# Kernel optimization log

Hardware: AMD Instinct MI355X
Metric: run time of the kernel (lower is better)

Reference implementation:

```python
import jax, jax.numpy as jnp
import numpy as np

N, LT, LV, D, H = 4, 1024, 1024, 1024, 16
HD = D // H
EPS = 1e-12


def layernorm(x, w, b):
    u = x.mean(-1, keepdims=True)
    s = ((x - u) ** 2).mean(-1, keepdims=True)
    return w * (x - u) / jnp.sqrt(s + EPS) + b


def attention(q_in, k_in, v_in, mask, qw, qb, kw, kb, vw, vb):
    # mask: (N, Lq_or_1, Lk) float in {0,1}; torch Linear is x @ W.T + b
    def heads(x, w, b):
        y = x @ w.T + b
        return y.reshape(y.shape[0], y.shape[1], H, HD).transpose(0, 2, 1, 3)  # (N,H,L,hd)
    q, k, v = heads(q_in, qw, qb), heads(k_in, kw, kb), heads(v_in, vw, vb)
    scores = jnp.einsum('bhqd,bhkd->bhqk', q, k) / np.sqrt(HD).astype(np.float32)
    scores = scores + (1.0 - mask[:, None]) * (-10000.0)
    probs = jax.nn.softmax(scores, axis=-1)  # dropout is identity in eval
    ctx = jnp.einsum('bhqk,bhkd->bhqd', probs, v)
    return ctx.transpose(0, 2, 1, 3).reshape(q_in.shape[0], q_in.shape[1], D)


def setup_inputs() -> dict:
    key = jax.random.key(0)
    ks = jax.random.split(key, 16)
    inp = {
        'dec_hidden_states': jax.random.normal(ks[0], (N, LT, D), jnp.float32),
        'enc_outputs': jax.random.normal(ks[1], (N, LV, D), jnp.float32),
        'dec_mask': jnp.ones((N, LT), jnp.float32),
        'enc_mask': jnp.ones((N, LV), jnp.float32),
    }
    wnames = ['sa_qw', 'sa_kw', 'sa_vw', 'ca_qw', 'ca_kw', 'ca_vw', 'out_w']
    for i, n in enumerate(wnames):
        inp[n] = jax.random.normal(ks[2 + i], (D, D), jnp.float32) * 0.02
    for n in ['sa_qb', 'sa_kb', 'sa_vb', 'ca_qb', 'ca_kb', 'ca_vb', 'out_b', 'n1_b', 'n2_b', 'out_ln_b']:
        inp[n] = jnp.zeros((D,), jnp.float32)
    for n in ['n1_w', 'n2_w', 'out_ln_w']:
        inp[n] = jnp.ones((D,), jnp.float32)
    return inp


def reference(dec_hidden_states, enc_outputs, dec_mask, enc_mask,
              sa_qw, sa_qb, sa_kw, sa_kb, sa_vw, sa_vb, n1_w, n1_b,
              ca_qw, ca_qb, ca_kw, ca_kb, ca_vw, ca_vb, n2_w, n2_b,
              out_w, out_b, out_ln_w, out_ln_b):
    Lt = dec_mask.shape[1]
    # diagonal_mask=True: causal tril combined with padding mask
    self_mask = dec_mask[:, None, :] * jnp.tril(jnp.ones((Lt, Lt), dec_mask.dtype))  # (N,Lt,Lt)
    a = attention(dec_hidden_states, dec_hidden_states, dec_hidden_states, self_mask,
                  sa_qw, sa_qb, sa_kw, sa_kb, sa_vw, sa_vb)
    a = layernorm(a + dec_hidden_states, n1_w, n1_b)
    c = attention(a, enc_outputs, enc_outputs, enc_mask[:, None, :],
                  ca_qw, ca_qb, ca_kw, ca_kb, ca_vw, ca_vb)
    c = layernorm(a + c, n2_w, n2_b)
    # BertOutput called as output(x, x): dense, residual, LN (dropout = identity)
    h = c @ out_w.T + out_b
    return layernorm(h + c, out_ln_w, out_ln_b)
```

## Files before the change

kernel.cpp:

```cpp
#include <hip/hip_runtime.h>
#include <cstdint>
#include <cstddef>

typedef __bf16 bf16x8 __attribute__((ext_vector_type(8)));
typedef float  floatx4 __attribute__((ext_vector_type(4)));
typedef unsigned short ushortx8 __attribute__((ext_vector_type(8)));
typedef unsigned short ushortx4 __attribute__((ext_vector_type(4)));

#define MFMA16(a, b, c) __builtin_amdgcn_mfma_f32_16x16x32_bf16((a), (b), (c), 0, 0, 0)

__device__ inline unsigned short f2bf(float f) {
    unsigned int u = __float_as_uint(f);
    unsigned int r = (u + 0x7fffu + ((u >> 16) & 1u)) >> 16;
    return (unsigned short)r;
}

struct Src2 { const float* p[2]; };
__global__ __launch_bounds__(256) void k_x2_to_bf16(Src2 s2, unsigned short* __restrict__ dst) {
    int i = blockIdx.x * 256 + threadIdx.x;
    const float* src = s2.p[i >> 19];
    int off = i & 524287;
    const float4* s = (const float4*)src + (size_t)off * 2;
    float4 x0 = s[0], x1 = s[1];
    ushortx8 o;
    o[0] = f2bf(x0.x); o[1] = f2bf(x0.y); o[2] = f2bf(x0.z); o[3] = f2bf(x0.w);
    o[4] = f2bf(x1.x); o[5] = f2bf(x1.y); o[6] = f2bf(x1.z); o[7] = f2bf(x1.w);
    *((ushortx8*)dst + i) = o;
}
struct Src7 { const float* p[7]; };
__global__ __launch_bounds__(256) void k_w7_to_bf16(Src7 s7, unsigned short* __restrict__ dst) {
    int i = blockIdx.x * 256 + threadIdx.x;
    const float* src = s7.p[i >> 17];
    int off = i & 131071;
    const float4* s = (const float4*)src + (size_t)off * 2;
    float4 x0 = s[0], x1 = s[1];
    ushortx8 o;
    o[0] = f2bf(x0.x); o[1] = f2bf(x0.y); o[2] = f2bf(x0.z); o[3] = f2bf(x0.w);
    o[4] = f2bf(x1.x); o[5] = f2bf(x1.y); o[6] = f2bf(x1.z); o[7] = f2bf(x1.w);
    *((ushortx8*)dst + i) = o;
}

template <int MODE>
__global__ __launch_bounds__(256) void k_gemm_bias(const unsigned short* __restrict__ A,
                                                   const unsigned short* __restrict__ A2,
                                                   const unsigned short* __restrict__ W,
                                                   const float* __restrict__ bias0,
                                                   const float* __restrict__ bias1,
                                                   const float* __restrict__ bias2,
                                                   void* __restrict__ d0,
                                                   void* __restrict__ d1,
                                                   void* __restrict__ d2,
                                                   int K) {
    __shared__ __align__(16) unsigned short As[128 * 32];
    __shared__ __align__(16) unsigned short Bs[128 * 32];
    const int tid = threadIdx.x;
    const int wave = tid >> 6, lane = tid & 63;
    const int quad = lane >> 4, l15 = lane & 15;
    const int wm = wave >> 1, wn = wave & 1;
    const int m0 = blockIdx.x * 128, n0 = blockIdx.y * 128;
    const int sect_blk = n0 >> 10;

    const unsigned short* Ause = (MODE == 4 && sect_blk != 0) ? A2 : A;

    const size_t rowbytes = (size_t)K * 2;
    const int idx0 = tid, idx1 = 256 + tid;
    const int rA0 = idx0 >> 2, cb0 = (idx0 & 3) << 4;
    const int rA1 = idx1 >> 2, cb1 = (idx1 & 3) << 4;
    const char* gA0 = (const char*)Ause + (size_t)(m0 + rA0) * rowbytes + cb0;
    const char* gA1 = (const char*)Ause + (size_t)(m0 + rA1) * rowbytes + cb1;
    const char* gB0 = (const char*)W + (size_t)(n0 + rA0) * rowbytes + cb0;
    const char* gB1 = (const char*)W + (size_t)(n0 + rA1) * rowbytes + cb1;

    int4 pa0 = *(const int4*)gA0, pa1 = *(const int4*)gA1;
    int4 pb0 = *(const int4*)gB0, pb1 = *(const int4*)gB1;

    floatx4 acc[4][4] = {};

    const int KT = K >> 5;
    for (int kt = 0; kt < KT; ++kt) {
        __syncthreads();
        ((int4*)As)[idx0] = pa0; ((int4*)As)[idx1] = pa1;
        ((int4*)Bs)[idx0] = pb0; ((int4*)Bs)[idx1] = pb1;
        __syncthreads();
        if (kt + 1 < KT) {
            gA0 += 64; gA1 += 64; gB0 += 64; gB1 += 64;
            pa0 = *(const int4*)gA0; pa1 = *(const int4*)gA1;
            pb0 = *(const int4*)gB0; pb1 = *(const int4*)gB1;
        }
        bf16x8 af[4], bfr[4];
        const char* Asb = (const char*)As;
        const char* Bsb = (const char*)Bs;
#pragma unroll
        for (int r = 0; r < 4; ++r)
            af[r] = *(const bf16x8*)(Asb + ((wm * 64 + r * 16 + l15) * 64 + quad * 16));
#pragma unroll
        for (int c = 0; c < 4; ++c)
            bfr[c] = *(const bf16x8*)(Bsb + ((wn * 64 + c * 16 + l15) * 64 + quad * 16));
#pragma unroll
        for (int r = 0; r < 4; ++r)
#pragma unroll
            for (int c = 0; c < 4; ++c)
                acc[r][c] = MFMA16(af[r], bfr[c], acc[r][c]);
    }

#pragma unroll
    for (int c = 0; c < 4; ++c) {
        int col = n0 + wn * 64 + c * 16 + l15;
        int sect = col >> 10, cc = col & 1023;
        float bv;
        if (MODE == 3) bv = bias0[col];
        else bv = (sect == 0 ? bias0 : (sect == 1 ? bias1 : bias2))[cc];
        int h = cc >> 6, d = cc & 63;
#pragma unroll
        for (int r = 0; r < 4; ++r) {
            int mrow = m0 + wm * 64 + r * 16 + quad * 4;
#pragma unroll
            for (int i = 0; i < 4; ++i) {
                float v = acc[r][c][i] + bv;
                int row = mrow + i;
                if (MODE == 3) {
                    ((float*)d0)[(size_t)row * 1024 + col] = v;
                } else {
                    int b = row >> 10, l = row & 1023;
                    unsigned short* base = (unsigned short*)(sect == 0 ? d0 : (sect == 1 ? d1 : d2));
                    bool isV = (sect == 2);
                    size_t off;
                    if (isV) {
                        int kk = l & 31;
                        int kperm = ((kk & 15) << 1) | (kk >> 4);
                        off = (size_t)(b * 16 + h) * 65536 + (size_t)(l >> 5) * 2048 + d * 32 + kperm;
                    } else {
                        off = ((size_t)(b * 16 + h) * 1024 + l) * 64 + d;
                    }
                    base[off] = f2bf(v);
                }
            }
        }
    }
}

__global__ __launch_bounds__(256, 2) void k_flash_attn(const unsigned short* __restrict__ Qp,
                                                       const unsigned short* __restrict__ Kp,
                                                       const unsigned short* __restrict__ Vp,
                                                       const float* __restrict__ mask,
                                                       float* __restrict__ ctx,
                                                       int causal) {
    const int L = 1024, D = 1024;
    const float SC = 0.18033688011112042f;
    int f = blockIdx.x;
    int g = f >> 6;
    int bh = (f & 7) + (g << 3);
    int qt = ((f >> 3) + g) & 7;
    int h = bh & 15, b = bh >> 4;
    int tid = threadIdx.x;
    int wave = tid >> 6, lane = tid & 63, quad = lane >> 4, l15 = lane & 15;
    int qbase = qt * 128 + wave * 32;

    __shared__ __align__(16) unsigned short Ks[4096];
    __shared__ __align__(16) unsigned short Vs[5120];
    __shared__ float penf[1024];
    __shared__ __align__(16) unsigned short Plds[4 * 1280];

    {
        float4 mv = ((const float4*)(mask + b * L))[tid];
        float4 pv;
        pv.x = (1.0f - mv.x) * -14426.950408889634f;
        pv.y = (1.0f - mv.y) * -14426.950408889634f;
        pv.z = (1.0f - mv.z) * -14426.950408889634f;
        pv.w = (1.0f - mv.w) * -14426.950408889634f;
        ((float4*)penf)[tid] = pv;
    }

    const unsigned short* Qh = Qp + ((size_t)(b * 16 + h) * 1024 + qbase) * 64;
    bf16x8 qf[2][2];
#pragma unroll
    for (int qh = 0; qh < 2; ++qh) {
        qf[qh][0] = *(const bf16x8*)(Qh + (qh * 16 + l15) * 64 + quad * 8);
        qf[qh][1] = *(const bf16x8*)(Qh + (qh * 16 + l15) * 64 + 32 + quad * 8);
    }

    const char* Kh = (const char*)(Kp + (size_t)(b * 16 + h) * 65536);
    const char* Vh = (const char*)(Vp + (size_t)(b * 16 + h) * 65536);

    int ktiles = causal ? (2 * qt + 2) : 16;

    char* Ksb = (char*)Ks;
    char* Vsb = (char*)Vs;
    int krow = tid >> 3, kblk = tid & 7;
    int kd0 = krow * 128 + ((kblk ^ (krow & 7)) << 4);
    int kd1 = kd0 + 32 * 128;
    int vd0 = (tid >> 2) * 80 + ((tid & 3) << 4);
    int vd1 = vd0 + 5120;

    int karA[4], karB[4];
#pragma unroll
    for (int r = 0; r < 4; ++r) {
        int row = r * 16 + l15;
        karA[r] = row * 128 + ((quad ^ (l15 & 7)) << 4);
        karB[r] = row * 128 + (((quad | 4) ^ (l15 & 7)) << 4);
    }
    int var_[8];
#pragma unroll
    for (int s = 0; s < 2; ++s)
#pragma unroll
        for (int fi = 0; fi < 4; ++fi)
            var_[s * 4 + fi] = s * 5120 + (fi * 16 + l15) * 80 + (quad << 4);

    floatx4 O[2][4] = {};
    float lsum[2][4] = {};
    unsigned short* pw = &Plds[wave * 1280];
    unsigned int* pw32 = (unsigned int*)pw;

    int4 ka0 = *(const int4*)(Kh + tid * 16);
    int4 ka1 = *(const int4*)(Kh + 4096 + tid * 16);
    int4 va0 = *(const int4*)(Vh + tid * 16);
    int4 va1 = *(const int4*)(Vh + 4096 + tid * 16);

    for (int kt = 0; kt < ktiles; ++kt) {
        *(int4*)(Ksb + kd0) = ka0;
        *(int4*)(Ksb + kd1) = ka1;
        *(int4*)(Vsb + vd0) = va0;
        *(int4*)(Vsb + vd1) = va1;
        __syncthreads();
        if (kt + 1 < ktiles) {
            const char* Kg = Kh + (size_t)(kt + 1) * 8192;
            const char* Vg = Vh + (size_t)(kt + 1) * 8192;
            ka0 = *(const int4*)(Kg + tid * 16);
            ka1 = *(const int4*)(Kg + 4096 + tid * 16);
            va0 = *(const int4*)(Vg + tid * 16);
            va1 = *(const int4*)(Vg + 4096 + tid * 16);
        }
        int k0 = kt * 64;

        if (!(causal && k0 > qbase + 31)) {
            bf16x8 kA[4], kB[4];
#pragma unroll
            for (int r = 0; r < 4; ++r) {
                kA[r] = *(const bf16x8*)(Ksb + karA[r]);
                kB[r] = *(const bf16x8*)(Ksb + karB[r]);
            }
            bf16x8 vv[8];
#pragma unroll
            for (int s = 0; s < 8; ++s) vv[s] = *(const bf16x8*)(Vsb + var_[s]);
            float pr0 = penf[k0 + l15];
            float pr1 = penf[k0 + 16 + l15];
            float pr2 = penf[k0 + 32 + l15];
            float pr3 = penf[k0 + 48 + l15];

#pragma unroll
            for (int qh = 0; qh < 2; ++qh) {
                int qlo = qbase + qh * 16;
                if (causal && k0 > qlo + 15) continue;
                bool boundary = causal && (k0 + 63 > qlo);

                floatx4 S0 = {}, S1 = {}, S2 = {}, S3 = {};
                S0 = MFMA16(qf[qh][0], kA[0], S0); S0 = MFMA16(qf[qh][1], kB[0], S0);
                S1 = MFMA16(qf[qh][0], kA[1], S1); S1 = MFMA16(qf[qh][1], kB[1], S1);
                S2 = MFMA16(qf[qh][0], kA[2], S2); S2 = MFMA16(qf[qh][1], kB[2], S2);
                S3 = MFMA16(qf[qh][0], kA[3], S3); S3 = MFMA16(qf[qh][1], kB[3], S3);

                int qrow = qlo + quad * 4;
#pragma unroll
                for (int i = 0; i < 4; ++i) {
                    float x0 = fmaf(S0[i], SC, pr0);
                    float x1 = fmaf(S1[i], SC, pr1);
                    float x2 = fmaf(S2[i], SC, pr2);
                    float x3 = fmaf(S3[i], SC, pr3);
                    if (boundary) {
                        int q = qrow + i;
                        x0 = ((k0 + l15) <= q) ? x0 : -50000.0f;
                        x1 = ((k0 + 16 + l15) <= q) ? x1 : -50000.0f;
                        x2 = ((k0 + 32 + l15) <= q) ? x2 : -50000.0f;
                        x3 = ((k0 + 48 + l15) <= q) ? x3 : -50000.0f;
                    }
                    float p0 = __builtin_amdgcn_exp2f(x0);
                    float p1 = __builtin_amdgcn_exp2f(x1);
                    float p2 = __builtin_amdgcn_exp2f(x2);
                    float p3 = __builtin_amdgcn_exp2f(x3);
                    lsum[qh][i] += (p0 + p1) + (p2 + p3);
                    unsigned r0 = __float_as_uint(p0) + 0x8000u;
                    unsigned r1 = __float_as_uint(p1) + 0x8000u;
                    unsigned r2 = __float_as_uint(p2) + 0x8000u;
                    unsigned r3 = __float_as_uint(p3) + 0x8000u;
                    unsigned plo = __builtin_amdgcn_perm(r1, r0, 0x07060302u);
                    unsigned phi = __builtin_amdgcn_perm(r3, r2, 0x07060302u);
                    int ro = (quad * 4 + i) * 20;
                    pw32[ro + l15] = plo;
                    pw32[320 + ro + l15] = phi;
                }
                bf16x8 pa_lo = *(const bf16x8*)(pw + l15 * 40 + quad * 8);
                bf16x8 pa_hi = *(const bf16x8*)(pw + 640 + l15 * 40 + quad * 8);
                O[qh][0] = MFMA16(pa_lo, vv[0], O[qh][0]);
                O[qh][1] = MFMA16(pa_lo, vv[1], O[qh][1]);
                O[qh][2] = MFMA16(pa_lo, vv[2], O[qh][2]);
                O[qh][3] = MFMA16(pa_lo, vv[3], O[qh][3]);
                O[qh][0] = MFMA16(pa_hi, vv[4], O[qh][0]);
                O[qh][1] = MFMA16(pa_hi, vv[5], O[qh][1]);
                O[qh][2] = MFMA16(pa_hi, vv[6], O[qh][2]);
                O[qh][3] = MFMA16(pa_hi, vv[7], O[qh][3]);
            }
        }
        __syncthreads();
    }

#pragma unroll
    for (int qh = 0; qh < 2; ++qh)
#pragma unroll
        for (int i = 0; i < 4; ++i) {
            float l = lsum[qh][i];
            l += __shfl_xor(l, 1);
            l += __shfl_xor(l, 2);
            l += __shfl_xor(l, 4);
            l += __shfl_xor(l, 8);
            float inv = 1.0f / l;
            int q = qbase + qh * 16 + quad * 4 + i;
            float* op = ctx + ((size_t)(b * L + q)) * D + h * 64;
#pragma unroll
            for (int fi = 0; fi < 4; ++fi) op[fi * 16 + l15] = O[qh][fi][i] * inv;
        }
}

__global__ __launch_bounds__(256) void k_add_ln(const float* __restrict__ X,
                                                const float* __restrict__ Y,
                                                const float* __restrict__ w,
                                                const float* __restrict__ bvec,
                                                float* __restrict__ outf,
                                                unsigned short* __restrict__ outbf) {
    int row = blockIdx.x;
    int tid = threadIdx.x;
    float4 x = *((const float4*)(X + (size_t)row * 1024) + tid);
    float4 y = *((const float4*)(Y + (size_t)row * 1024) + tid);
    float v0 = x.x + y.x, v1 = x.y + y.y, v2 = x.z + y.z, v3 = x.w + y.w;
    float s = v0 + v1 + v2 + v3;
    float s2 = v0 * v0 + v1 * v1 + v2 * v2 + v3 * v3;
#pragma unroll
    for (int off = 32; off > 0; off >>= 1) {
        s += __shfl_xor(s, off);
        s2 += __shfl_xor(s2, off);
    }
    __shared__ float red[8];
    int wave = tid >> 6, lane = tid & 63;
    if (lane == 0) { red[wave] = s; red[4 + wave] = s2; }
    __syncthreads();
    s = red[0] + red[1] + red[2] + red[3];
    s2 = red[4] + red[5] + red[6] + red[7];
    float u = s * (1.0f / 1024.0f);
    float var = s2 * (1.0f / 1024.0f) - u * u;
    float r = 1.0f / sqrtf(fmaxf(var, 0.0f) + 1e-12f);
    float4 wv = *((const float4*)w + tid);
    float4 bv = *((const float4*)bvec + tid);
    float o0 = wv.x * (v0 - u) * r + bv.x;
    float o1 = wv.y * (v1 - u) * r + bv.y;
    float o2 = wv.z * (v2 - u) * r + bv.z;
    float o3 = wv.w * (v3 - u) * r + bv.w;
    float4 o = {o0, o1, o2, o3};
    *((float4*)(outf + (size_t)row * 1024) + tid) = o;
    if (outbf) {
        ushortx4 ob;
        ob[0] = f2bf(o0); ob[1] = f2bf(o1); ob[2] = f2bf(o2); ob[3] = f2bf(o3);
        *((ushortx4*)outbf + (size_t)row * 256 + tid) = ob;
    }
}

extern "C" void kernel_launch(void* const* d_in, const int* in_sizes, int n_in,
                              void* d_out, int out_size, void* d_ws, size_t ws_size,
                              hipStream_t stream) {
    (void)in_sizes; (void)n_in; (void)out_size; (void)ws_size;
    const float* dec = (const float*)d_in[0];
    const float* enc = (const float*)d_in[1];
    const float* dec_mask = (const float*)d_in[2];
    const float* enc_mask = (const float*)d_in[3];
    const float* b_saq = (const float*)d_in[11];
    const float* b_sak = (const float*)d_in[12];
    const float* b_sav = (const float*)d_in[13];
    const float* b_caq = (const float*)d_in[14];
    const float* b_cak = (const float*)d_in[15];
    const float* b_cav = (const float*)d_in[16];
    const float* b_out = (const float*)d_in[17];
    const float* n1_b = (const float*)d_in[18];
    const float* n2_b = (const float*)d_in[19];
    const float* oln_b = (const float*)d_in[20];
    const float* n1_w = (const float*)d_in[21];
    const float* n2_w = (const float*)d_in[22];
    const float* oln_w = (const float*)d_in[23];

    char* ws = (char*)d_ws;
    const size_t MB2 = 2097152;
    const size_t ACT_BF = 8388608;
    const size_t ACT_F32 = 16777216;
    unsigned short* Wbf[7];
    for (int i = 0; i < 7; ++i) Wbf[i] = (unsigned short*)(ws + i * MB2);
    size_t off = 7 * MB2;
    unsigned short* Xbf = (unsigned short*)(ws + off); off += ACT_BF;
    unsigned short* Ebf = (unsigned short*)(ws + off); off += ACT_BF;
    unsigned short* Abf = (unsigned short*)(ws + off); off += ACT_BF;
    unsigned short* Cbf = (unsigned short*)(ws + off); off += ACT_BF;
    unsigned short* Qp = (unsigned short*)(ws + off); off += ACT_BF;
    unsigned short* Kp = (unsigned short*)(ws + off); off += ACT_BF;
    unsigned short* Vp = (unsigned short*)(ws + off); off += ACT_BF;
    float* ctx = (float*)(ws + off); off += ACT_F32;
    float* a_f32 = (float*)(ws + off); off += ACT_F32;
    float* c_f32 = (float*)(ws + off); off += ACT_F32;
    float* h_f32 = ctx;
    float* outp = (float*)d_out;

    dim3 blk(256);
    dim3 attn_grid(512);

    Src2 s2; s2.p[0] = dec; s2.p[1] = enc;
    k_x2_to_bf16<<<dim3(4096), blk, 0, stream>>>(s2, Xbf);
    Src7 s7;
    for (int i = 0; i < 7; ++i) s7.p[i] = (const float*)d_in[4 + i];
    k_w7_to_bf16<<<dim3(3584), blk, 0, stream>>>(s7, Wbf[0]);

    k_gemm_bias<0><<<dim3(32, 24), blk, 0, stream>>>(Xbf, Xbf, Wbf[0], b_saq, b_sak, b_sav,
                                                     Qp, Kp, Vp, 1024);
    k_flash_attn<<<attn_grid, blk, 0, stream>>>(Qp, Kp, Vp, dec_mask, ctx, 1);
    k_add_ln<<<dim3(4096), blk, 0, stream>>>(ctx, dec, n1_w, n1_b, a_f32, Abf);

    k_gemm_bias<4><<<dim3(32, 24), blk, 0, stream>>>(Abf, Ebf, Wbf[3], b_caq, b_cak, b_cav,
                                                     Qp, Kp, Vp, 1024);
    k_flash_attn<<<attn_grid, blk, 0, stream>>>(Qp, Kp, Vp, enc_mask, ctx, 0);
    k_add_ln<<<dim3(4096), blk, 0, stream>>>(a_f32, ctx, n2_w, n2_b, c_f32, Cbf);

    k_gemm_bias<3><<<dim3(32, 8), blk, 0, stream>>>(Cbf, Cbf, Wbf[6], b_out, b_out, b_out,
                                                    h_f32, nullptr, nullptr, 1024);
    k_add_ln<<<dim3(4096), blk, 0, stream>>>(h_f32, c_f32, oln_w, oln_b, outp, (unsigned short*)nullptr);
}
```

Baseline: 337.6 us.

## Double GEMM K-tile to 64 and remap blocks for XCD-local L2 reuse

The GEMM K step per shared-memory stage grows from 32 to 64, which halves the number of barrier pairs per output tile and doubles the prefetched global loads in flight. Each block's flat id is also remapped so that blocks landing on the same XCD (id mod 8) share the same M rows and sweep across N tiles, aiming for better L2 reuse of A and W. In exchange it uses more LDS and registers per block, which may lower occupancy. The remap also hard-codes grid shapes (32 in x, 8 or 24 N tiles) that have to match the launch configuration.

```diff
diff --git a/kernel.cpp b/kernel.cpp
--- a/kernel.cpp
+++ b/kernel.cpp
@@ -51,56 +51,69 @@
                                                    void* __restrict__ d1,
                                                    void* __restrict__ d2,
                                                    int K) {
-    __shared__ __align__(16) unsigned short As[128 * 32];
-    __shared__ __align__(16) unsigned short Bs[128 * 32];
+    __shared__ __align__(16) unsigned short As[128 * 64];
+    __shared__ __align__(16) unsigned short Bs[128 * 64];
     const int tid = threadIdx.x;
     const int wave = tid >> 6, lane = tid & 63;
     const int quad = lane >> 4, l15 = lane & 15;
     const int wm = wave >> 1, wn = wave & 1;
-    const int m0 = blockIdx.x * 128, n0 = blockIdx.y * 128;
+
+    constexpr int NT = (MODE == 3) ? 8 : 24;
+    int fid = blockIdx.y * 32 + blockIdx.x;
+    int xcd = fid & 7, idx = fid >> 3;
+    const int m0 = (xcd * 4 + idx / NT) * 128;
+    const int n0 = (idx % NT) * 128;
     const int sect_blk = n0 >> 10;
 
     const unsigned short* Ause = (MODE == 4 && sect_blk != 0) ? A2 : A;
 
     const size_t rowbytes = (size_t)K * 2;
     const int idx0 = tid, idx1 = 256 + tid;
-    const int rA0 = idx0 >> 2, cb0 = (idx0 & 3) << 4;
-    const int rA1 = idx1 >> 2, cb1 = (idx1 & 3) << 4;
-    const char* gA0 = (const char*)Ause + (size_t)(m0 + rA0) * rowbytes + cb0;
-    const char* gA1 = (const char*)Ause + (size_t)(m0 + rA1) * rowbytes + cb1;
-    const char* gB0 = (const char*)W + (size_t)(n0 + rA0) * rowbytes + cb0;
-    const char* gB1 = (const char*)W + (size_t)(n0 + rA1) * rowbytes + cb1;
-
-    int4 pa0 = *(const int4*)gA0, pa1 = *(const int4*)gA1;
-    int4 pb0 = *(const int4*)gB0, pb1 = *(const int4*)gB1;
+    const char* pA0 = (const char*)Ause + (size_t)(m0 + (idx0 >> 2)) * rowbytes + ((idx0 & 3) << 4);
+    const char* pA1 = (const char*)Ause + (size_t)(m0 + (idx1 >> 2)) * rowbytes + ((idx1 & 3) << 4);
+    const char* pB0 = (const char*)W + (size_t)(n0 + (idx0 >> 2)) * rowbytes + ((idx0 & 3) << 4);
+    const char* pB1 = (const char*)W + (size_t)(n0 + (idx1 >> 2)) * rowbytes + ((idx1 & 3) << 4);
+
+    int4 a0a = *(const int4*)pA0, a0b = *(const int4*)(pA0 + 64);
+    int4 a1a = *(const int4*)pA1, a1b = *(const int4*)(pA1 + 64);
+    int4 b0a = *(const int4*)pB0, b0b = *(const int4*)(pB0 + 64);
+    int4 b1a = *(const int4*)pB1, b1b = *(const int4*)(pB1 + 64);
 
     floatx4 acc[4][4] = {};
 
-    const int KT = K >> 5;
+    const int KT = K >> 6;
     for (int kt = 0; kt < KT; ++kt) {
         __syncthreads();
-        ((int4*)As)[idx0] = pa0; ((int4*)As)[idx1] = pa1;
-        ((int4*)Bs)[idx0] = pb0; ((int4*)Bs)[idx1] = pb1;
+        ((int4*)As)[idx0] = a0a; ((int4*)As)[idx1] = a1a;
+        ((int4*)As)[512 + idx0] = a0b; ((int4*)As)[512 + idx1] = a1b;
+        ((int4*)Bs)[idx0] = b0a; ((int4*)Bs)[idx1] = b1a;
+        ((int4*)Bs)[512 + idx0] = b0b; ((int4*)Bs)[512 + idx1] = b1b;
         __syncthreads();
         if (kt + 1 < KT) {
-            gA0 += 64; gA1 += 64; gB0 += 64; gB1 += 64;
-            pa0 = *(const int4*)gA0; pa1 = *(const int4*)gA1;
-            pb0 = *(const int4*)gB0; pb1 = *(const int4*)gB1;
-        }
-        bf16x8 af[4], bfr[4];
+            pA0 += 128; pA1 += 128; pB0 += 128; pB1 += 128;
+            a0a = *(const int4*)pA0; a0b = *(const int4*)(pA0 + 64);
+            a1a = *(const int4*)pA1; a1b = *(const int4*)(pA1 + 64);
+            b0a = *(const int4*)pB0; b0b = *(const int4*)(pB0 + 64);
+            b1a = *(const int4*)pB1; b1b = *(const int4*)(pB1 + 64);
+        }
         const char* Asb = (const char*)As;
         const char* Bsb = (const char*)Bs;
 #pragma unroll
-        for (int r = 0; r < 4; ++r)
-            af[r] = *(const bf16x8*)(Asb + ((wm * 64 + r * 16 + l15) * 64 + quad * 16));
-#pragma unroll
-        for (int c = 0; c < 4; ++c)
-            bfr[c] = *(const bf16x8*)(Bsb + ((wn * 64 + c * 16 + l15) * 64 + quad * 16));
-#pragma unroll
-        for (int r = 0; r < 4; ++r)
+        for (int half = 0; half < 2; ++half) {
+            const int hb = half * 8192;
+            bf16x8 af[4], bfr[4];
+#pragma unroll
+            for (int r = 0; r < 4; ++r)
+                af[r] = *(const bf16x8*)(Asb + hb + ((wm * 64 + r * 16 + l15) * 64 + quad * 16));
 #pragma unroll
             for (int c = 0; c < 4; ++c)
-                acc[r][c] = MFMA16(af[r], bfr[c], acc[r][c]);
+                bfr[c] = *(const bf16x8*)(Bsb + hb + ((wn * 64 + c * 16 + l15) * 64 + quad * 16));
+#pragma unroll
+            for (int r = 0; r < 4; ++r)
+#pragma unroll
+                for (int c = 0; c < 4; ++c)
+                    acc[r][c] = MFMA16(af[r], bfr[c], acc[r][c]);
+        }
     }
 
 #pragma unroll
```

After: 331.1 us. Within noise of the previous version (-1.9%).
